# Optimization experiments

Hardware: AMD Instinct MI355X
Metric: run time of the kernel (lower is better)

## Reference

```python
import jax, jax.numpy as jnp
import numpy as np

# BoeNet deterministic (greedy) BFS rollout reference.
# Assumptions (source truncated): GrowthPolicyNet ~ Linear(H,1)+sigmoid applied to
# node hidden + DEPTH_EMBED_SCALE * depth_embedding; greedy path expands when
# prob > greedy_threshold. Tree is materialized as a complete binary tree up to
# max_depth with per-node active masks (jit-friendly; honors data-dependent growth
# via masking instead of dynamic shapes). Pooling: mean over active nodes.

V, E, H = 32000, 512, 512
MAX_DEPTH = 3
DEPTH_EMBED_SCALE = 0.01
GREEDY_THRESHOLD = 0.5
PROB_MIN, PROB_MAX = 1e-7, 1.0 - 1e-7
EPS = 1e-8
SIB_SCALE = 1.0 / np.sqrt(H)


def setup_inputs() -> dict:
    key = jax.random.key(0)
    ks = jax.random.split(key, 8)
    B, S = 8, 512
    return {
        "tokens": jax.random.randint(ks[0], (B, S), 0, V),
        "emb": jax.random.normal(ks[1], (V, E), jnp.float32) * 0.02,
        "Wp": jax.random.normal(ks[2], (E, H), jnp.float32) / np.sqrt(E),
        "bp": jnp.zeros((H,), jnp.float32),
        "Wc": jax.random.normal(ks[3], (H, 2 * H), jnp.float32) / np.sqrt(H),
        "bc": jnp.zeros((2 * H,), jnp.float32),
        "Wg": jax.random.normal(ks[4], (H, 1), jnp.float32) / np.sqrt(H),
        "bg": jnp.zeros((1,), jnp.float32),
        "dep": jax.random.normal(ks[5], (MAX_DEPTH + 1, H), jnp.float32) * 0.01,
        "sib": jax.random.normal(ks[6], (2, H), jnp.float32) * 0.02,
        "Wout": jax.random.normal(ks[7], (H, V), jnp.float32) / np.sqrt(H),
        "bout": jnp.zeros((V,), jnp.float32),
    }


def reference(tokens, emb, Wp, bp, Wc, bc, Wg, bg, dep, sib, Wout, bout):
    B, S = tokens.shape
    N = B * S
    # h0: embedding lookup + projection, flattened to positions [N, H]
    h0 = (emb[tokens.reshape(N)] @ Wp + bp)  # [N, H]

    nodes = h0[:, None, :]                    # [N, 1, H] level-0 nodes
    active = jnp.ones((N, 1), h0.dtype)
    agg_sum = h0                              # root always counted
    agg_count = jnp.ones((N,), h0.dtype)

    for d in range(MAX_DEPTH):
        n = nodes.shape[1]
        # growth policy: sigmoid gate on node hidden + scaled depth embedding
        gate_in = nodes + DEPTH_EMBED_SCALE * dep[d]
        prob = jax.nn.sigmoid(jnp.einsum('nkh,ho->nko', gate_in, Wg)[..., 0] + bg[0])
        prob = jnp.clip(prob, PROB_MIN, PROB_MAX)           # [N, n]
        expand = (prob > GREEDY_THRESHOLD).astype(h0.dtype) * active  # [N, n]
        # children: Linear(H, 2H) split into left/right, plus sibling embeddings
        ch = (jnp.einsum('nkh,hj->nkj', nodes, Wc) + bc).reshape(N, 2 * n, H)
        sib_idx = jnp.tile(jnp.arange(2), n)                # [0,1,0,1,...]
        ch = ch + SIB_SCALE * sib[sib_idx]
        ch_active = jnp.repeat(expand, 2, axis=1)           # [N, 2n]
        agg_sum = agg_sum + jnp.einsum('nkh,nk->nh', ch, ch_active)
        agg_count = agg_count + ch_active.sum(axis=1)
        nodes, active = ch, ch_active

    pooled = agg_sum / jnp.maximum(agg_count, EPS)[:, None]  # mean pooling
    logits = pooled @ Wout + bout                            # [N, V]
    return logits.reshape(B, S, V)
```

## Files before the change

kernel.cpp:

```cpp
#include <hip/hip_runtime.h>
#include <cstdint>

#define BM 128
#define BN 128
#define BK 32

typedef __attribute__((ext_vector_type(8))) short short8;
typedef _Float16 half8 __attribute__((ext_vector_type(8)));
typedef __attribute__((ext_vector_type(4))) float floatx4;

union H8 { short8 s; half8 h; };

static constexpr float SIBS   = 0.044194173824159216f;
static constexpr float LS_INV = 1.0f / 2048.0f;

__device__ __forceinline__ unsigned short f2bf(float x){
    union { float f; unsigned u32; } v; v.f = x;
    unsigned r = ((v.u32 >> 16) & 1u) + 0x7fffu;
    return (unsigned short)((v.u32 + r) >> 16);
}
__device__ __forceinline__ void split_f16(float x, unsigned short& h, unsigned short& s){
    _Float16 hh = (_Float16)x;
    _Float16 ss = (_Float16)((x - (float)hh) * 2048.0f);
    union { _Float16 f; unsigned short u; } a, b;
    a.f = hh; b.f = ss;
    h = a.u; s = b.u;
}

#define GLDS(g, l) __builtin_amdgcn_global_load_lds( \
    (const __attribute__((address_space(1))) void*)(g), \
    (__attribute__((address_space(3))) void*)(l), 16, 0, 0)

__global__ void prep_split16_T(const float* __restrict__ src,
                               unsigned short* __restrict__ hiT,
                               unsigned short* __restrict__ lsT,
                               int R, int C)
{
    __shared__ float t[32][33];
    int c0 = blockIdx.x * 32, r0 = blockIdx.y * 32;
    int tx = threadIdx.x & 31, ty = threadIdx.x >> 5;
#pragma unroll
    for (int k = 0; k < 4; k++){
        int r = ty + k*8;
        t[r][tx] = src[(size_t)(r0 + r) * C + c0 + tx];
    }
    __syncthreads();
#pragma unroll
    for (int k = 0; k < 4; k++){
        int r = ty + k*8;
        float x = t[tx][r];
        unsigned short h, s;
        split_f16(x, h, s);
        size_t o = (size_t)(c0 + r) * R + r0 + tx;
        hiT[o] = h; lsT[o] = s;
    }
}

__global__ void prep_wc2_T(const float* __restrict__ Wc,
                           unsigned short* __restrict__ hiT,
                           unsigned short* __restrict__ lsT)
{
    __shared__ float t[32][33];
    int c0 = blockIdx.x * 32, r0 = blockIdx.y * 32;
    int tx = threadIdx.x & 31, ty = threadIdx.x >> 5;
#pragma unroll
    for (int k = 0; k < 4; k++){
        int r = ty + k*8;
        t[r][tx] = Wc[(size_t)(r0 + r) * 1024 + c0 + tx]
                 + Wc[(size_t)(r0 + r) * 1024 + 512 + c0 + tx];
    }
    __syncthreads();
#pragma unroll
    for (int k = 0; k < 4; k++){
        int r = ty + k*8;
        float x = t[tx][r];
        unsigned short h, s;
        split_f16(x, h, s);
        size_t o = (size_t)(c0 + r) * 512 + r0 + tx;
        hiT[o] = h; lsT[o] = s;
    }
}

__global__ void prep_bf16_T(const float* __restrict__ src,
                            unsigned short* __restrict__ dstT,
                            int R, int C)
{
    __shared__ float t[32][33];
    int c0 = blockIdx.x * 32, r0 = blockIdx.y * 32;
    int tx = threadIdx.x & 31, ty = threadIdx.x >> 5;
#pragma unroll
    for (int k = 0; k < 4; k++){
        int r = ty + k*8;
        t[r][tx] = src[(size_t)(r0 + r) * C + c0 + tx];
    }
    __syncthreads();
#pragma unroll
    for (int k = 0; k < 4; k++){
        int r = ty + k*8;
        dstT[(size_t)(c0 + r) * R + r0 + tx] = f2bf(t[tx][r]);
    }
}

template<int MODE, int DEPTH>
__global__ __launch_bounds__(256, 2)
void gemm_k(const unsigned short* __restrict__ Abf,
            const unsigned short* __restrict__ Agh,
            const unsigned short* __restrict__ Agl,
            const unsigned short* __restrict__ BTh,
            const unsigned short* __restrict__ BTl,
            const float* __restrict__ bias,
            const int* __restrict__ tokens,
            const float* __restrict__ emb,
            const float* __restrict__ sib,
            const float* __restrict__ mArr,
            const float* __restrict__ cinv,
            const float* __restrict__ h0,
            float* __restrict__ nodes_next,
            unsigned short* __restrict__ nxh,
            unsigned short* __restrict__ nxl,
            float* __restrict__ f32out,
            unsigned short* __restrict__ pooled,
            float* __restrict__ out,
            int N)
{
    constexpr int K = 512;
    __shared__ __align__(16) unsigned short Ah[BM*BK];
    __shared__ __align__(16) unsigned short Al[BM*BK];
    __shared__ __align__(16) unsigned short Bh[BK*BN];
    __shared__ __align__(16) unsigned short Bl[BK*BN];

    const int tid = threadIdx.x;
    const int w = tid >> 6, l = tid & 63;
    const int wr = w >> 1, wc = w & 1;
    const int row0 = blockIdx.x * BM;
    const int n0   = blockIdx.y * BN;
    const int q = l >> 4, lm = l & 15;

    floatx4 acc[4][4]  = {};
    floatx4 accx[4][4] = {};

    const float* aptr = nullptr;
    const int am = tid & 127, kq0 = tid >> 7;
    if (MODE == 0) aptr = emb + (long)tokens[row0 + am] * K;

    long arow0 = 0, arow1 = 0;
    if (MODE != 0){
        arow0 = (long)(row0 + l) * K;
        arow1 = (long)(row0 + 64 + l) * K;
    }
    const long brow0 = (long)(n0 + l) * K;
    const long brow1 = (long)(n0 + 64 + l) * K;

    for (int k0 = 0; k0 < K; k0 += BK){
        __syncthreads();
        GLDS(BTh + brow0 + k0 + w*8, (char*)Bh + w*2048);
        GLDS(BTh + brow1 + k0 + w*8, (char*)Bh + w*2048 + 1024);
        if (MODE != 2){
            GLDS(BTl + brow0 + k0 + w*8, (char*)Bl + w*2048);
            GLDS(BTl + brow1 + k0 + w*8, (char*)Bl + w*2048 + 1024);
        }
        if (MODE == 1 || MODE == 3){
            GLDS(Agh + arow0 + k0 + w*8, (char*)Ah + w*2048);
            GLDS(Agh + arow1 + k0 + w*8, (char*)Ah + w*2048 + 1024);
            GLDS(Agl + arow0 + k0 + w*8, (char*)Al + w*2048);
            GLDS(Agl + arow1 + k0 + w*8, (char*)Al + w*2048 + 1024);
        } else if (MODE == 2){
            GLDS(Abf + arow0 + k0 + w*8, (char*)Ah + w*2048);
            GLDS(Abf + arow1 + k0 + w*8, (char*)Ah + w*2048 + 1024);
        } else {
#pragma unroll
            for (int t = 0; t < 2; t++){
                int kq = kq0 + 2*t;
                const float* src = aptr + k0 + kq*8;
                float xs[8];
                *(floatx4*)&xs[0] = *(const floatx4*)(src);
                *(floatx4*)&xs[4] = *(const floatx4*)(src + 4);
                unsigned short h8[8], l8[8];
#pragma unroll
                for (int e = 0; e < 8; e++) split_f16(xs[e], h8[e], l8[e]);
                int s = kq*128 + am;
                *(short8*)&Ah[s*8] = *(const short8*)h8;
                *(short8*)&Al[s*8] = *(const short8*)l8;
            }
        }
        __syncthreads();

        H8 bh[4], bl[4];
#pragma unroll
        for (int j = 0; j < 4; j++){
            bh[j].s = *(const short8*)&Bh[(q*128 + wc*64 + j*16 + lm)*8];
            if (MODE != 2)
                bl[j].s = *(const short8*)&Bl[(q*128 + wc*64 + j*16 + lm)*8];
        }
#pragma unroll
        for (int i = 0; i < 4; i++){
            H8 ah; ah.s = *(const short8*)&Ah[(q*128 + wr*64 + i*16 + lm)*8];
            if (MODE != 2){
                H8 al; al.s = *(const short8*)&Al[(q*128 + wr*64 + i*16 + lm)*8];
#pragma unroll
                for (int j = 0; j < 4; j++)
                    acc[i][j]  = __builtin_amdgcn_mfma_f32_16x16x32_f16(ah.h, bh[j].h, acc[i][j], 0, 0, 0);
#pragma unroll
                for (int j = 0; j < 4; j++)
                    accx[i][j] = __builtin_amdgcn_mfma_f32_16x16x32_f16(ah.h, bl[j].h, accx[i][j], 0, 0, 0);
#pragma unroll
                for (int j = 0; j < 4; j++)
                    accx[i][j] = __builtin_amdgcn_mfma_f32_16x16x32_f16(al.h, bh[j].h, accx[i][j], 0, 0, 0);
            } else {
#pragma unroll
                for (int j = 0; j < 4; j++)
                    acc[i][j] = __builtin_amdgcn_mfma_f32_16x16x32_bf16(ah.s, bh[j].s, acc[i][j], 0, 0, 0);
            }
        }
    }

#pragma unroll
    for (int i = 0; i < 4; i++){
        int rbase = row0 + wr*64 + i*16 + q*4;
#pragma unroll
        for (int j = 0; j < 4; j++){
            int col = n0 + wc*64 + j*16 + lm;
            float badd = 0.f, bsum = 0.f;
            int half = 0, h = 0;
            if (MODE == 0 || MODE == 2) badd = bias[col];
            if (MODE == 1){
                half = col >> 9; h = col & 511;
                badd = bias[col] + SIBS * sib[half*512 + h];
            }
            if (MODE == 3)
                bsum = bias[col] + bias[512 + col] + SIBS * (sib[col] + sib[512 + col]);
#pragma unroll
            for (int r = 0; r < 4; r++){
                int row = rbase + r;
                float v = acc[i][j][r];
                if (MODE != 2) v += accx[i][j][r] * LS_INV;
                if (MODE == 0){
                    v += badd;
                    long o = (long)row*512 + col;
                    f32out[o] = v;
                    unsigned short hh, ss; split_f16(v, hh, ss);
                    nxh[o] = hh; nxl[o] = ss;
                } else if (MODE == 1){
                    v += badd;
                    long o = (long)(2*row + half)*512 + h;
                    nodes_next[o] = v;
                    if (DEPTH == 0){
                        unsigned short hh, ss; split_f16(v, hh, ss);
                        nxh[o] = hh; nxl[o] = ss;
                    }
                } else if (MODE == 3){
                    long o = (long)row*512 + col;
                    float outv = (h0[o] + v + mArr[row]*bsum) * cinv[row];
                    pooled[o] = f2bf(outv);
                } else {
                    out[(long)row*(long)N + col] = v + badd;
                }
            }
        }
    }
}

__global__ void gate_k(const float* __restrict__ nodes,
                       const float* __restrict__ Wg,
                       const float* __restrict__ bg,
                       const float* __restrict__ deprow,
                       const unsigned char* __restrict__ eprev,
                       unsigned char* __restrict__ e,
                       int depth)
{
    int row = blockIdx.x * 4 + (threadIdx.x >> 6);
    int l = threadIdx.x & 63;
    const float* nr = nodes + (long)row * 512;
    float s = 0.f;
#pragma unroll
    for (int t = 0; t < 8; t++){
        int h = t*64 + l;
        s += (nr[h] + 0.01f * deprow[h]) * Wg[h];
    }
#pragma unroll
    for (int off = 32; off > 0; off >>= 1) s += __shfl_down(s, off);
    if (l == 0){
        float x = s + bg[0];
        unsigned char a = (depth == 0) ? (unsigned char)1 : eprev[row >> 1];
        e[row] = (unsigned char)((x > 0.f) && a);
    }
}

__global__ void msum_k(const float* __restrict__ nodes0,
                       const float* __restrict__ nodes1,
                       const float* __restrict__ nodes2,
                       const unsigned char* __restrict__ e0,
                       const unsigned char* __restrict__ e1,
                       const unsigned char* __restrict__ e2,
                       unsigned short* __restrict__ Sh,
                       unsigned short* __restrict__ Sl,
                       float* __restrict__ mArr,
                       float* __restrict__ cinv)
{
    int n = blockIdx.x;
    float a0  = (float)e0[n];
    float a10 = (float)e1[2*n],   a11 = (float)e1[2*n+1];
    float a20 = (float)e2[4*n],   a21 = (float)e2[4*n+1];
    float a22 = (float)e2[4*n+2], a23 = (float)e2[4*n+3];
    if (threadIdx.x == 0){
        float m = a0 + a10 + a11 + a20 + a21 + a22 + a23;
        mArr[n] = m;
        cinv[n] = 1.f / (1.f + 2.f * m);
    }
    const float* p0 = nodes0 + (long)n * 512;
    const float* p1 = nodes1 + (long)(2*n) * 512;
    const float* p2 = nodes2 + (long)(4*n) * 512;
    for (int c = threadIdx.x; c < 512; c += 256){
        float s = a0 * p0[c]
                + a10 * p1[c]        + a11 * p1[512 + c]
                + a20 * p2[c]        + a21 * p2[512 + c]
                + a22 * p2[1024 + c] + a23 * p2[1536 + c];
        unsigned short hh, ss; split_f16(s, hh, ss);
        long o = (long)n * 512 + c;
        Sh[o] = hh; Sl[o] = ss;
    }
}

extern "C" void kernel_launch(void* const* d_in, const int* in_sizes, int n_in,
                              void* d_out, int out_size, void* d_ws, size_t ws_size,
                              hipStream_t stream)
{
    const int*   tokens = (const int*)d_in[0];
    const float* emb    = (const float*)d_in[1];
    const float* Wp     = (const float*)d_in[2];
    const float* bp     = (const float*)d_in[3];
    const float* Wc     = (const float*)d_in[4];
    const float* bc     = (const float*)d_in[5];
    const float* Wg     = (const float*)d_in[6];
    const float* bg     = (const float*)d_in[7];
    const float* dep    = (const float*)d_in[8];
    const float* sib    = (const float*)d_in[9];
    const float* Wout   = (const float*)d_in[10];
    const float* bout   = (const float*)d_in[11];

    if (ws_size < ((size_t)48 << 20)) return;

    char* w = (char*)d_ws;
    auto alloc = [&](size_t bytes)->char*{
        char* p = w; w += (bytes + 255) & ~(size_t)255; return p;
    };
    unsigned short* WpT_h  = (unsigned short*)alloc((size_t)512*512*2);
    unsigned short* WpT_l  = (unsigned short*)alloc((size_t)512*512*2);
    unsigned short* WcT_h  = (unsigned short*)alloc((size_t)1024*512*2);
    unsigned short* WcT_l  = (unsigned short*)alloc((size_t)1024*512*2);
    unsigned short* Wc2T_h = (unsigned short*)alloc((size_t)512*512*2);
    unsigned short* Wc2T_l = (unsigned short*)alloc((size_t)512*512*2);
    unsigned short* WoutT  = (unsigned short*)alloc((size_t)32000*512*2);
    unsigned short* pooled = (unsigned short*)alloc((size_t)4096*512*2);
    unsigned char*  e0     = (unsigned char*)alloc(4096);
    unsigned char*  e1     = (unsigned char*)alloc(8192);
    unsigned char*  e2     = (unsigned char*)alloc(16384);

    char* ob = (char*)d_out;
    float*          nodes0 = (float*)(ob + ((size_t) 64 << 20));
    unsigned short* n0h    = (unsigned short*)(ob + ((size_t) 80 << 20));
    unsigned short* n0l    = (unsigned short*)(ob + ((size_t) 88 << 20));
    float*          nodes1 = (float*)(ob + ((size_t) 96 << 20));
    unsigned short* n1h    = (unsigned short*)(ob + ((size_t)128 << 20));
    unsigned short* n1l    = (unsigned short*)(ob + ((size_t)144 << 20));
    float*          nodes2 = (float*)(ob + ((size_t)160 << 20));
    unsigned short* Sh     = (unsigned short*)(ob + ((size_t)200 << 20));
    unsigned short* Sl     = (unsigned short*)(ob + ((size_t)208 << 20));
    float*          mArr   = (float*)(ob + ((size_t)216 << 20));
    float*          cinvA  = (float*)(ob + ((size_t)217 << 20));
    float*          out    = (float*)d_out;

    prep_split16_T<<<dim3(16, 16),   256, 0, stream>>>(Wp, WpT_h, WpT_l, 512, 512);
    prep_split16_T<<<dim3(32, 16),   256, 0, stream>>>(Wc, WcT_h, WcT_l, 512, 1024);
    prep_wc2_T    <<<dim3(16, 16),   256, 0, stream>>>(Wc, Wc2T_h, Wc2T_l);
    prep_bf16_T   <<<dim3(1000, 16), 256, 0, stream>>>(Wout, WoutT, 512, 32000);

    gemm_k<0,0><<<dim3(32, 4), 256, 0, stream>>>(nullptr, nullptr, nullptr,
        WpT_h, WpT_l, bp, tokens, emb, nullptr, nullptr, nullptr, nullptr,
        nullptr, n0h, n0l, nodes0, nullptr, nullptr, 512);

    gate_k<<<1024, 256, 0, stream>>>(nodes0, Wg, bg, dep + 0, nullptr, e0, 0);

    gemm_k<1,0><<<dim3(32, 8), 256, 0, stream>>>(nullptr, n0h, n0l,
        WcT_h, WcT_l, bc, nullptr, nullptr, sib, nullptr, nullptr, nullptr,
        nodes1, n1h, n1l, nullptr, nullptr, nullptr, 1024);

    gate_k<<<2048, 256, 0, stream>>>(nodes1, Wg, bg, dep + 512, e0, e1, 1);

    gemm_k<1,1><<<dim3(64, 8), 256, 0, stream>>>(nullptr, n1h, n1l,
        WcT_h, WcT_l, bc, nullptr, nullptr, sib, nullptr, nullptr, nullptr,
        nodes2, nullptr, nullptr, nullptr, nullptr, nullptr, 1024);

    gate_k<<<4096, 256, 0, stream>>>(nodes2, Wg, bg, dep + 1024, e1, e2, 2);

    msum_k<<<4096, 256, 0, stream>>>(nodes0, nodes1, nodes2, e0, e1, e2,
        Sh, Sl, mArr, cinvA);

    gemm_k<3,0><<<dim3(32, 4), 256, 0, stream>>>(nullptr, Sh, Sl,
        Wc2T_h, Wc2T_l, bc, nullptr, nullptr, sib, mArr, cinvA, nodes0,
        nullptr, nullptr, nullptr, nullptr, pooled, nullptr, 512);

    gemm_k<2,0><<<dim3(32, 250), 256, 0, stream>>>(pooled, nullptr, nullptr,
        WoutT, nullptr, bout, nullptr, nullptr, nullptr, nullptr, nullptr, nullptr,
        nullptr, nullptr, nullptr, nullptr, nullptr, out, 32000);
}
```

Measured before the change: 1.008 ms.

## Double-buffer LDS tiles to overlap global loads with MFMA compute

```diff
diff --git a/kernel.cpp b/kernel.cpp
--- a/kernel.cpp
+++ b/kernel.cpp
@@ -124,10 +124,11 @@
             int N)
 {
     constexpr int K = 512;
-    __shared__ __align__(16) unsigned short Ah[BM*BK];
-    __shared__ __align__(16) unsigned short Al[BM*BK];
-    __shared__ __align__(16) unsigned short Bh[BK*BN];
-    __shared__ __align__(16) unsigned short Bl[BK*BN];
+    constexpr int TS = BM * BK;
+    __shared__ __align__(16) unsigned short Ah[2*TS];
+    __shared__ __align__(16) unsigned short Bh[2*TS];
+    __shared__ __align__(16) unsigned short Al[(MODE==2) ? 8 : 2*TS];
+    __shared__ __align__(16) unsigned short Bl[(MODE==2) ? 8 : 2*TS];
 
     const int tid = threadIdx.x;
     const int w = tid >> 6, l = tid & 63;
@@ -151,52 +152,78 @@
     const long brow0 = (long)(n0 + l) * K;
     const long brow1 = (long)(n0 + 64 + l) * K;
 
-    for (int k0 = 0; k0 < K; k0 += BK){
-        __syncthreads();
-        GLDS(BTh + brow0 + k0 + w*8, (char*)Bh + w*2048);
-        GLDS(BTh + brow1 + k0 + w*8, (char*)Bh + w*2048 + 1024);
-        if (MODE != 2){
-            GLDS(BTl + brow0 + k0 + w*8, (char*)Bl + w*2048);
-            GLDS(BTl + brow1 + k0 + w*8, (char*)Bl + w*2048 + 1024);
-        }
-        if (MODE == 1 || MODE == 3){
-            GLDS(Agh + arow0 + k0 + w*8, (char*)Ah + w*2048);
-            GLDS(Agh + arow1 + k0 + w*8, (char*)Ah + w*2048 + 1024);
-            GLDS(Agl + arow0 + k0 + w*8, (char*)Al + w*2048);
-            GLDS(Agl + arow1 + k0 + w*8, (char*)Al + w*2048 + 1024);
-        } else if (MODE == 2){
-            GLDS(Abf + arow0 + k0 + w*8, (char*)Ah + w*2048);
-            GLDS(Abf + arow1 + k0 + w*8, (char*)Ah + w*2048 + 1024);
-        } else {
-#pragma unroll
-            for (int t = 0; t < 2; t++){
-                int kq = kq0 + 2*t;
-                const float* src = aptr + k0 + kq*8;
-                float xs[8];
-                *(floatx4*)&xs[0] = *(const floatx4*)(src);
-                *(floatx4*)&xs[4] = *(const floatx4*)(src + 4);
-                unsigned short h8[8], l8[8];
-#pragma unroll
-                for (int e = 0; e < 8; e++) split_f16(xs[e], h8[e], l8[e]);
-                int s = kq*128 + am;
-                *(short8*)&Ah[s*8] = *(const short8*)h8;
-                *(short8*)&Al[s*8] = *(const short8*)l8;
-            }
-        }
-        __syncthreads();
-
+#define STAGE_TILE(buf, kk)                                                  \
+    {                                                                        \
+        char* bhp = (char*)Bh + (buf)*8192 + w*2048;                         \
+        GLDS(BTh + brow0 + (kk) + w*8, bhp);                                 \
+        GLDS(BTh + brow1 + (kk) + w*8, bhp + 1024);                         \
+        if (MODE != 2){                                                      \
+            char* blp = (char*)Bl + (buf)*8192 + w*2048;                     \
+            GLDS(BTl + brow0 + (kk) + w*8, blp);                             \
+            GLDS(BTl + brow1 + (kk) + w*8, blp + 1024);                     \
+        }                                                                    \
+        if (MODE == 1 || MODE == 3){                                         \
+            char* ahp = (char*)Ah + (buf)*8192 + w*2048;                     \
+            char* alp = (char*)Al + (buf)*8192 + w*2048;                     \
+            GLDS(Agh + arow0 + (kk) + w*8, ahp);                             \
+            GLDS(Agh + arow1 + (kk) + w*8, ahp + 1024);                     \
+            GLDS(Agl + arow0 + (kk) + w*8, alp);                             \
+            GLDS(Agl + arow1 + (kk) + w*8, alp + 1024);                     \
+        } else if (MODE == 2){                                               \
+            char* ahp = (char*)Ah + (buf)*8192 + w*2048;                     \
+            GLDS(Abf + arow0 + (kk) + w*8, ahp);                             \
+            GLDS(Abf + arow1 + (kk) + w*8, ahp + 1024);                     \
+        }                                                                    \
+    }
+
+    STAGE_TILE(0, 0);
+    if (MODE == 0){
+#pragma unroll
+        for (int tt = 0; tt < 2; tt++){
+            int kq = kq0 + 2*tt;
+            const float* src = aptr + kq*8;
+            float xs[8];
+            *(floatx4*)&xs[0] = *(const floatx4*)(src);
+            *(floatx4*)&xs[4] = *(const floatx4*)(src + 4);
+            unsigned short h8[8], l8[8];
+#pragma unroll
+            for (int e = 0; e < 8; e++) split_f16(xs[e], h8[e], l8[e]);
+            int s = kq*128 + am;
+            *(short8*)&Ah[s*8] = *(const short8*)h8;
+            *(short8*)&Al[s*8] = *(const short8*)l8;
+        }
+    }
+    __syncthreads();
+
+    constexpr int nIter = K / BK;
+    for (int t = 0; t < nIter; t++){
+        const int cur = t & 1, nxt = cur ^ 1;
+        const bool more = (t + 1 < nIter);
+        const int knext = (t + 1) * BK;
+
+        if (more) STAGE_TILE(nxt, knext);
+
+        floatx4 pA0, pA1, pA2, pA3;
+        if (MODE == 0 && more){
+            const float* s0 = aptr + knext + kq0*8;
+            const float* s1 = aptr + knext + (kq0+2)*8;
+            pA0 = *(const floatx4*)(s0); pA1 = *(const floatx4*)(s0 + 4);
+            pA2 = *(const floatx4*)(s1); pA3 = *(const floatx4*)(s1 + 4);
+        }
+
+        const int off = cur * TS;
         H8 bh[4], bl[4];
 #pragma unroll
         for (int j = 0; j < 4; j++){
-            bh[j].s = *(const short8*)&Bh[(q*128 + wc*64 + j*16 + lm)*8];
+            bh[j].s = *(const short8*)&Bh[off + (q*128 + wc*64 + j*16 + lm)*8];
             if (MODE != 2)
-                bl[j].s = *(const short8*)&Bl[(q*128 + wc*64 + j*16 + lm)*8];
+                bl[j].s = *(const short8*)&Bl[off + (q*128 + wc*64 + j*16 + lm)*8];
         }
 #pragma unroll
         for (int i = 0; i < 4; i++){
-            H8 ah; ah.s = *(const short8*)&Ah[(q*128 + wr*64 + i*16 + lm)*8];
+            H8 ah; ah.s = *(const short8*)&Ah[off + (q*128 + wr*64 + i*16 + lm)*8];
             if (MODE != 2){
-                H8 al; al.s = *(const short8*)&Al[(q*128 + wr*64 + i*16 + lm)*8];
+                H8 al; al.s = *(const short8*)&Al[off + (q*128 + wr*64 + i*16 + lm)*8];
 #pragma unroll
                 for (int j = 0; j < 4; j++)
                     acc[i][j]  = __builtin_amdgcn_mfma_f32_16x16x32_f16(ah.h, bh[j].h, acc[i][j], 0, 0, 0);
@@ -212,7 +239,26 @@
                     acc[i][j] = __builtin_amdgcn_mfma_f32_16x16x32_bf16(ah.s, bh[j].s, acc[i][j], 0, 0, 0);
             }
         }
-    }
+
+        if (MODE == 0 && more){
+            float xs[8];
+            unsigned short h8[8], l8[8];
+            *(floatx4*)&xs[0] = pA0; *(floatx4*)&xs[4] = pA1;
+#pragma unroll
+            for (int e = 0; e < 8; e++) split_f16(xs[e], h8[e], l8[e]);
+            int s = kq0*128 + am;
+            *(short8*)&Ah[nxt*TS + s*8] = *(const short8*)h8;
+            *(short8*)&Al[nxt*TS + s*8] = *(const short8*)l8;
+            *(floatx4*)&xs[0] = pA2; *(floatx4*)&xs[4] = pA3;
+#pragma unroll
+            for (int e = 0; e < 8; e++) split_f16(xs[e], h8[e], l8[e]);
+            s = (kq0+2)*128 + am;
+            *(short8*)&Ah[nxt*TS + s*8] = *(const short8*)h8;
+            *(short8*)&Al[nxt*TS + s*8] = *(const short8*)l8;
+        }
+        __syncthreads();
+    }
+#undef STAGE_TILE
 
 #pragma unroll
     for (int i = 0; i < 4; i++){
```

New measurement: 1.015 ms. No clear change (+0.7%).

## Fuse gate dot products into GEMM epilogues, merge prep kernels, swizzle output GEMM

Applied to the files above, without the earlier changes.

```diff
diff --git a/kernel.cpp b/kernel.cpp
--- a/kernel.cpp
+++ b/kernel.cpp
@@ -31,73 +31,67 @@
     (const __attribute__((address_space(1))) void*)(g), \
     (__attribute__((address_space(3))) void*)(l), 16, 0, 0)
 
-__global__ void prep_split16_T(const float* __restrict__ src,
-                               unsigned short* __restrict__ hiT,
-                               unsigned short* __restrict__ lsT,
-                               int R, int C)
+__global__ void prep_all(const float* __restrict__ Wp, const float* __restrict__ Wc,
+                         const float* __restrict__ Wout, const float* __restrict__ Wg,
+                         const float* __restrict__ bg, const float* __restrict__ dep,
+                         unsigned short* __restrict__ WpT_h, unsigned short* __restrict__ WpT_l,
+                         unsigned short* __restrict__ WcT_h, unsigned short* __restrict__ WcT_l,
+                         unsigned short* __restrict__ Wc2T_h, unsigned short* __restrict__ Wc2T_l,
+                         unsigned short* __restrict__ WoutT,
+                         float* __restrict__ gacc, float* __restrict__ cgate)
 {
+    int bid = blockIdx.x;
+    if (bid >= 17024){
+        if (bid < 17032){
+            int base = (bid - 17024)*3584 + threadIdx.x;
+#pragma unroll
+            for (int k = 0; k < 14; k++) gacc[base + k*256] = 0.f;
+        } else {
+            int wv = threadIdx.x >> 6, l = threadIdx.x & 63;
+            if (wv < 3){
+                float s = 0.f;
+#pragma unroll
+                for (int t = 0; t < 8; t++){
+                    int h = t*64 + l;
+                    s += dep[wv*512 + h] * Wg[h];
+                }
+#pragma unroll
+                for (int off = 32; off > 0; off >>= 1) s += __shfl_down(s, off);
+                if (l == 0) cgate[wv] = 0.01f*s + bg[0];
+            }
+        }
+        return;
+    }
     __shared__ float t[32][33];
-    int c0 = blockIdx.x * 32, r0 = blockIdx.y * 32;
+    const float* src = nullptr;
+    unsigned short *dh = nullptr, *dl = nullptr;
+    int C = 512, bx, by; bool sum2 = false;
+    if (bid < 256){ src=Wp; dh=WpT_h; dl=WpT_l; C=512; bx=bid&15; by=bid>>4; }
+    else if (bid < 768){ int rel=bid-256; src=Wc; dh=WcT_h; dl=WcT_l; C=1024; bx=rel&31; by=rel>>5; }
+    else if (bid < 1024){ int rel=bid-768; src=Wc; dh=Wc2T_h; dl=Wc2T_l; C=512; sum2=true; bx=rel&15; by=rel>>4; }
+    else { int rel=bid-1024; src=Wout; dh=WoutT; dl=nullptr; C=32000; bx=rel%1000; by=rel/1000; }
+    int c0 = bx*32, r0 = by*32;
     int tx = threadIdx.x & 31, ty = threadIdx.x >> 5;
 #pragma unroll
     for (int k = 0; k < 4; k++){
         int r = ty + k*8;
-        t[r][tx] = src[(size_t)(r0 + r) * C + c0 + tx];
+        float x;
+        if (sum2) x = Wc[(size_t)(r0+r)*1024 + c0+tx] + Wc[(size_t)(r0+r)*1024 + 512 + c0+tx];
+        else      x = src[(size_t)(r0+r)*C + c0+tx];
+        t[r][tx] = x;
     }
     __syncthreads();
 #pragma unroll
     for (int k = 0; k < 4; k++){
         int r = ty + k*8;
         float x = t[tx][r];
-        unsigned short h, s;
-        split_f16(x, h, s);
-        size_t o = (size_t)(c0 + r) * R + r0 + tx;
-        hiT[o] = h; lsT[o] = s;
-    }
-}
-
-__global__ void prep_wc2_T(const float* __restrict__ Wc,
-                           unsigned short* __restrict__ hiT,
-                           unsigned short* __restrict__ lsT)
-{
-    __shared__ float t[32][33];
-    int c0 = blockIdx.x * 32, r0 = blockIdx.y * 32;
-    int tx = threadIdx.x & 31, ty = threadIdx.x >> 5;
-#pragma unroll
-    for (int k = 0; k < 4; k++){
-        int r = ty + k*8;
-        t[r][tx] = Wc[(size_t)(r0 + r) * 1024 + c0 + tx]
-                 + Wc[(size_t)(r0 + r) * 1024 + 512 + c0 + tx];
-    }
-    __syncthreads();
-#pragma unroll
-    for (int k = 0; k < 4; k++){
-        int r = ty + k*8;
-        float x = t[tx][r];
-        unsigned short h, s;
-        split_f16(x, h, s);
-        size_t o = (size_t)(c0 + r) * 512 + r0 + tx;
-        hiT[o] = h; lsT[o] = s;
-    }
-}
-
-__global__ void prep_bf16_T(const float* __restrict__ src,
-                            unsigned short* __restrict__ dstT,
-                            int R, int C)
-{
-    __shared__ float t[32][33];
-    int c0 = blockIdx.x * 32, r0 = blockIdx.y * 32;
-    int tx = threadIdx.x & 31, ty = threadIdx.x >> 5;
-#pragma unroll
-    for (int k = 0; k < 4; k++){
-        int r = ty + k*8;
-        t[r][tx] = src[(size_t)(r0 + r) * C + c0 + tx];
-    }
-    __syncthreads();
-#pragma unroll
-    for (int k = 0; k < 4; k++){
-        int r = ty + k*8;
-        dstT[(size_t)(c0 + r) * R + r0 + tx] = f2bf(t[tx][r]);
+        size_t o = (size_t)(c0+r)*512 + r0+tx;
+        if (dl){
+            unsigned short h, s; split_f16(x, h, s);
+            dh[o] = h; dl[o] = s;
+        } else {
+            dh[o] = f2bf(x);
+        }
     }
 }
 
@@ -112,6 +106,8 @@
             const int* __restrict__ tokens,
             const float* __restrict__ emb,
             const float* __restrict__ sib,
+            const float* __restrict__ Wg,
+            float* __restrict__ gacc,
             const float* __restrict__ mArr,
             const float* __restrict__ cinv,
             const float* __restrict__ h0,
@@ -132,8 +128,17 @@
     const int tid = threadIdx.x;
     const int w = tid >> 6, l = tid & 63;
     const int wr = w >> 1, wc = w & 1;
-    const int row0 = blockIdx.x * BM;
-    const int n0   = blockIdx.y * BN;
+
+    int bx, by;
+    if (MODE == 2){
+        int bid = blockIdx.x;
+        int swz = (bid & 7) * 1000 + (bid >> 3);
+        bx = swz & 31; by = swz >> 5;
+    } else {
+        bx = blockIdx.x; by = blockIdx.y;
+    }
+    const int row0 = bx * BM;
+    const int n0   = by * BN;
     const int q = l >> 4, lm = l & 15;
 
     floatx4 acc[4][4]  = {};
@@ -214,19 +219,24 @@
         }
     }
 
+    float wgj[4];
+    if (MODE <= 1){
+#pragma unroll
+        for (int j = 0; j < 4; j++)
+            wgj[j] = Wg[(n0 + wc*64 + j*16 + lm) & 511];
+    }
+    const int halfc = n0 >> 9;
+
 #pragma unroll
     for (int i = 0; i < 4; i++){
         int rbase = row0 + wr*64 + i*16 + q*4;
+        float gp[4] = {0.f, 0.f, 0.f, 0.f};
 #pragma unroll
         for (int j = 0; j < 4; j++){
             int col = n0 + wc*64 + j*16 + lm;
             float badd = 0.f, bsum = 0.f;
-            int half = 0, h = 0;
             if (MODE == 0 || MODE == 2) badd = bias[col];
-            if (MODE == 1){
-                half = col >> 9; h = col & 511;
-                badd = bias[col] + SIBS * sib[half*512 + h];
-            }
+            if (MODE == 1) badd = bias[col] + SIBS * sib[halfc*512 + (col & 511)];
             if (MODE == 3)
                 bsum = bias[col] + bias[512 + col] + SIBS * (sib[col] + sib[512 + col]);
 #pragma unroll
@@ -236,13 +246,15 @@
                 if (MODE != 2) v += accx[i][j][r] * LS_INV;
                 if (MODE == 0){
                     v += badd;
+                    gp[r] += v * wgj[j];
                     long o = (long)row*512 + col;
                     f32out[o] = v;
                     unsigned short hh, ss; split_f16(v, hh, ss);
                     nxh[o] = hh; nxl[o] = ss;
                 } else if (MODE == 1){
                     v += badd;
-                    long o = (long)(2*row + half)*512 + h;
+                    gp[r] += v * wgj[j];
+                    long o = (long)(2*row + halfc)*512 + (col & 511);
                     nodes_next[o] = v;
                     if (DEPTH == 0){
                         unsigned short hh, ss; split_f16(v, hh, ss);
@@ -257,51 +269,49 @@
                 }
             }
         }
-    }
-}
-
-__global__ void gate_k(const float* __restrict__ nodes,
-                       const float* __restrict__ Wg,
-                       const float* __restrict__ bg,
-                       const float* __restrict__ deprow,
-                       const unsigned char* __restrict__ eprev,
-                       unsigned char* __restrict__ e,
-                       int depth)
-{
-    int row = blockIdx.x * 4 + (threadIdx.x >> 6);
-    int l = threadIdx.x & 63;
-    const float* nr = nodes + (long)row * 512;
-    float s = 0.f;
-#pragma unroll
-    for (int t = 0; t < 8; t++){
-        int h = t*64 + l;
-        s += (nr[h] + 0.01f * deprow[h]) * Wg[h];
-    }
-#pragma unroll
-    for (int off = 32; off > 0; off >>= 1) s += __shfl_down(s, off);
-    if (l == 0){
-        float x = s + bg[0];
-        unsigned char a = (depth == 0) ? (unsigned char)1 : eprev[row >> 1];
-        e[row] = (unsigned char)((x > 0.f) && a);
+        if (MODE <= 1){
+#pragma unroll
+            for (int r = 0; r < 4; r++){
+                float s = gp[r];
+                s += __shfl_xor(s, 1);
+                s += __shfl_xor(s, 2);
+                s += __shfl_xor(s, 4);
+                s += __shfl_xor(s, 8);
+                if (lm == 0){
+                    int row = rbase + r;
+                    int grow = (MODE == 0) ? row : (2*row + halfc);
+                    atomicAdd(&gacc[grow], s);
+                }
+            }
+        }
     }
 }
 
 __global__ void msum_k(const float* __restrict__ nodes0,
                        const float* __restrict__ nodes1,
                        const float* __restrict__ nodes2,
-                       const unsigned char* __restrict__ e0,
-                       const unsigned char* __restrict__ e1,
-                       const unsigned char* __restrict__ e2,
+                       const float* __restrict__ gacc,
+                       const float* __restrict__ cgate,
                        unsigned short* __restrict__ Sh,
                        unsigned short* __restrict__ Sl,
                        float* __restrict__ mArr,
                        float* __restrict__ cinv)
 {
     int n = blockIdx.x;
-    float a0  = (float)e0[n];
-    float a10 = (float)e1[2*n],   a11 = (float)e1[2*n+1];
-    float a20 = (float)e2[4*n],   a21 = (float)e2[4*n+1];
-    float a22 = (float)e2[4*n+2], a23 = (float)e2[4*n+3];
+    const float* g0 = gacc;
+    const float* g1 = gacc + 4096;
+    const float* g2 = gacc + 12288;
+    float c0 = cgate[0], c1 = cgate[1], c2 = cgate[2];
+    bool b0  =  g0[n]       + c0 > 0.f;
+    bool b10 = (g1[2*n]     + c1 > 0.f) && b0;
+    bool b11 = (g1[2*n + 1] + c1 > 0.f) && b0;
+    bool b20 = (g2[4*n]     + c2 > 0.f) && b10;
+    bool b21 = (g2[4*n + 1] + c2 > 0.f) && b10;
+    bool b22 = (g2[4*n + 2] + c2 > 0.f) && b11;
+    bool b23 = (g2[4*n + 3] + c2 > 0.f) && b11;
+    float a0  = (float)b0;
+    float a10 = (float)b10, a11 = (float)b11;
+    float a20 = (float)b20, a21 = (float)b21, a22 = (float)b22, a23 = (float)b23;
     if (threadIdx.x == 0){
         float m = a0 + a10 + a11 + a20 + a21 + a22 + a23;
         mArr[n] = m;
@@ -352,9 +362,8 @@
     unsigned short* Wc2T_l = (unsigned short*)alloc((size_t)512*512*2);
     unsigned short* WoutT  = (unsigned short*)alloc((size_t)32000*512*2);
     unsigned short* pooled = (unsigned short*)alloc((size_t)4096*512*2);
-    unsigned char*  e0     = (unsigned char*)alloc(4096);
-    unsigned char*  e1     = (unsigned char*)alloc(8192);
-    unsigned char*  e2     = (unsigned char*)alloc(16384);
+    float*          gacc   = (float*)alloc((size_t)28672*4);
+    float*          cgate  = (float*)alloc(256);
 
     char* ob = (char*)d_out;
     float*          nodes0 = (float*)(ob + ((size_t) 64 << 20));
@@ -370,37 +379,29 @@
     float*          cinvA  = (float*)(ob + ((size_t)217 << 20));
     float*          out    = (float*)d_out;
 
-    prep_split16_T<<<dim3(16, 16),   256, 0, stream>>>(Wp, WpT_h, WpT_l, 512, 512);
-    prep_split16_T<<<dim3(32, 16),   256, 0, stream>>>(Wc, WcT_h, WcT_l, 512, 1024);
-    prep_wc2_T    <<<dim3(16, 16),   256, 0, stream>>>(Wc, Wc2T_h, Wc2T_l);
-    prep_bf16_T   <<<dim3(1000, 16), 256, 0, stream>>>(Wout, WoutT, 512, 32000);
+    prep_all<<<17033, 256, 0, stream>>>(Wp, Wc, Wout, Wg, bg, dep,
+        WpT_h, WpT_l, WcT_h, WcT_l, Wc2T_h, Wc2T_l, WoutT, gacc, cgate);
 
     gemm_k<0,0><<<dim3(32, 4), 256, 0, stream>>>(nullptr, nullptr, nullptr,
-        WpT_h, WpT_l, bp, tokens, emb, nullptr, nullptr, nullptr, nullptr,
-        nullptr, n0h, n0l, nodes0, nullptr, nullptr, 512);
-
-    gate_k<<<1024, 256, 0, stream>>>(nodes0, Wg, bg, dep + 0, nullptr, e0, 0);
+        WpT_h, WpT_l, bp, tokens, emb, nullptr, Wg, gacc,
+        nullptr, nullptr, nullptr, nullptr, n0h, n0l, nodes0, nullptr, nullptr, 512);
 
     gemm_k<1,0><<<dim3(32, 8), 256, 0, stream>>>(nullptr, n0h, n0l,
-        WcT_h, WcT_l, bc, nullptr, nullptr, sib, nullptr, nullptr, nullptr,
-        nodes1, n1h, n1l, nullptr, nullptr, nullptr, 1024);
-
-    gate_k<<<2048, 256, 0, stream>>>(nodes1, Wg, bg, dep + 512, e0, e1, 1);
+        WcT_h, WcT_l, bc, nullptr, nullptr, sib, Wg, gacc + 4096,
+        nullptr, nullptr, nullptr, nodes1, n1h, n1l, nullptr, nullptr, nullptr, 1024);
 
     gemm_k<1,1><<<dim3(64, 8), 256, 0, stream>>>(nullptr, n1h, n1l,
-        WcT_h, WcT_l, bc, nullptr, nullptr, sib, nullptr, nullptr, nullptr,
-        nodes2, nullptr, nullptr, nullptr, nullptr, nullptr, 1024);
-
-    gate_k<<<4096, 256, 0, stream>>>(nodes2, Wg, bg, dep + 1024, e1, e2, 2);
-
-    msum_k<<<4096, 256, 0, stream>>>(nodes0, nodes1, nodes2, e0, e1, e2,
+        WcT_h, WcT_l, bc, nullptr, nullptr, sib, Wg, gacc + 12288,
+        nullptr, nullptr, nullptr, nodes2, nullptr, nullptr, nullptr, nullptr, nullptr, 1024);
+
+    msum_k<<<4096, 256, 0, stream>>>(nodes0, nodes1, nodes2, gacc, cgate,
         Sh, Sl, mArr, cinvA);
 
     gemm_k<3,0><<<dim3(32, 4), 256, 0, stream>>>(nullptr, Sh, Sl,
-        Wc2T_h, Wc2T_l, bc, nullptr, nullptr, sib, mArr, cinvA, nodes0,
-        nullptr, nullptr, nullptr, nullptr, pooled, nullptr, 512);
-
-    gemm_k<2,0><<<dim3(32, 250), 256, 0, stream>>>(pooled, nullptr, nullptr,
-        WoutT, nullptr, bout, nullptr, nullptr, nullptr, nullptr, nullptr, nullptr,
-        nullptr, nullptr, nullptr, nullptr, nullptr, out, 32000);
-}
+        Wc2T_h, Wc2T_l, bc, nullptr, nullptr, sib, nullptr, nullptr,
+        mArr, cinvA, nodes0, nullptr, nullptr, nullptr, nullptr, pooled, nullptr, 512);
+
+    gemm_k<2,0><<<dim3(8000), 256, 0, stream>>>(pooled, nullptr, nullptr,
+        WoutT, nullptr, bout, nullptr, nullptr, nullptr, nullptr, nullptr,
+        nullptr, nullptr, nullptr, nullptr, nullptr, nullptr, nullptr, nullptr, out, 32000);
+}
```

Result: no change. 1.003 ms (-0.4%).
